# Performance work log

Hardware: AMD Instinct MI355X
Metric: run time of the kernel (lower is better)

Reference implementation:

```python
import jax, jax.numpy as jnp
import numpy as np


def unfold(x, k, pad, stride):
    # x: [B, C, H, W] -> [B, C*k*k, L], matching torch.nn.functional.unfold
    B, C, H, W = x.shape
    p = jax.lax.conv_general_dilated_patches(
        x, (k, k), (stride, stride), [(pad, pad), (pad, pad)],
        dimension_numbers=("NCHW", "OIHW", "NCHW"))  # [B, C*k*k, Lh, Lw]
    return p.reshape(B, C * k * k, -1)


def fold(x, out_hw, k, pad, stride):
    # x: [B, C*k*k, L] -> [B, C, H, W] with overlap-add, matching F.fold
    B, F, L = x.shape
    C = F // (k * k)
    H, W = out_hw
    Hp, Wp = H + 2 * pad, W + 2 * pad
    Lh = (Hp - k) // stride + 1
    Lw = (Wp - k) // stride + 1
    v = x.reshape(B, C, k, k, Lh, Lw)
    rows = jnp.arange(k)[:, None] + jnp.arange(Lh)[None, :] * stride  # [k, Lh]
    cols = jnp.arange(k)[:, None] + jnp.arange(Lw)[None, :] * stride  # [k, Lw]
    idx = rows[:, None, :, None] * Wp + cols[None, :, None, :]        # [k, k, Lh, Lw]
    out = jnp.zeros((B, C, Hp * Wp), x.dtype)
    out = out.at[:, :, idx.reshape(-1)].add(v.reshape(B, C, -1))
    out = out.reshape(B, C, Hp, Wp)
    return out[:, :, pad:pad + H, pad:pad + W]


def setup_inputs() -> dict:
    key = jax.random.key(0)
    k1, k2, k3 = jax.random.split(key, 3)
    B, C, H, W = 2, 16, 96, 96
    return {
        "lrsr_lv1": jax.random.normal(k1, (B, C, H, W), jnp.float32),
        "refsr_lv1": jax.random.normal(k2, (B, C, H, W), jnp.float32),
        "org": jax.random.normal(k3, (B, C, 2 * H, 2 * W), jnp.float32),
        "kernel_size": 3,
        "padding": 1,
        "stride": 1,
        "lv": 2,
    }


def reference(lrsr_lv1, refsr_lv1, org, kernel_size, padding, stride, lv):
    k, pad, s = kernel_size, padding, stride
    eps = 1e-12  # F.normalize default eps
    lr_u = unfold(lrsr_lv1, k, pad, s)                       # [B, F, L]
    ref_u = unfold(refsr_lv1, k, pad, s).transpose(0, 2, 1)  # [B, L, F]
    ref_n = ref_u / jnp.maximum(
        jnp.sqrt(jnp.sum(ref_u * ref_u, axis=2, keepdims=True)), eps)
    lr_n = lr_u / jnp.maximum(
        jnp.sqrt(jnp.sum(lr_u * lr_u, axis=1, keepdims=True)), eps)
    R = jnp.einsum("blf,bfm->blm", ref_n, lr_n)              # [B, L_ref, L_lr]
    S = jnp.argmax(R, axis=1)                                 # [B, L_lr] int
    lv_ = max(lv - 1, 0)
    sc = 2 ** lv_
    k2, p2, s2 = sc * k, sc * pad, sc * s
    org_u = unfold(org, k2, p2, s2)                           # [B, F_org, L]
    T_u = jnp.take_along_axis(org_u, S[:, None, :], axis=2)   # bis gather
    H2 = lrsr_lv1.shape[2] * sc
    W2 = lrsr_lv1.shape[3] * sc
    T_org = fold(T_u, (H2, W2), k2, p2, s2)
    return T_org, S
```

## Files before the change

kernel.cpp:

```cpp
#include <hip/hip_runtime.h>
#include <float.h>


#define BATCH 2
#define CCH   16
#define HH    96
#define WW    96
#define LP    9216
#define KF    144
#define K3    160
#define OH    192
#define OW    192
#define NRT2  36
#define NCB2  36

typedef _Float16 f16;
typedef __attribute__((ext_vector_type(8))) _Float16 f16x8;
typedef __attribute__((ext_vector_type(4))) float    f32x4;

__device__ __forceinline__ void async16(const void* g, void* l) {
    __builtin_amdgcn_global_load_lds(
        (const __attribute__((address_space(1))) void*)g,
        (__attribute__((address_space(3))) void*)l, 16, 0, 0);
}

__global__ __launch_bounds__(256) void k_pack2(
        const float* __restrict__ ref, const float* __restrict__ lr,
        float* __restrict__ rinv, float* __restrict__ bns,
        f16* __restrict__ Abig, f16* __restrict__ Bbig) {
    __shared__ float imgS[CCH][3][26];
    __shared__ float pnorm[24][8];
    __shared__ float scl[24];
    int py = blockIdx.x, b = blockIdx.y;
    int side = blockIdx.z >> 2, q = blockIdx.z & 3;
    int tid = threadIdx.x;
    const float* img = (side ? lr : ref) + (size_t)b * CCH * HH * WW;

    for (int i = tid; i < CCH * 3 * 26; i += 256) {
        int c = i / 78, rem = i - c * 78;
        int rr = rem / 26, xx = rem - rr * 26;
        int y = py + rr - 1, xi = q * 24 - 1 + xx;
        float v = 0.f;
        if ((unsigned)y < (unsigned)HH && (unsigned)xi < (unsigned)WW)
            v = img[(c * HH + y) * WW + xi];
        imgS[c][rr][xx] = v;
    }
    __syncthreads();

    if (tid < 192) {
        int pxl = tid >> 3, part = tid & 7;
        float s = 0.f;
        #pragma unroll
        for (int cc = 0; cc < 2; ++cc) {
            int c = part * 2 + cc;
            #pragma unroll
            for (int dy = 0; dy < 3; ++dy)
                #pragma unroll
                for (int dx = 0; dx < 3; ++dx) {
                    float v = imgS[c][dy][pxl + dx];
                    s += v * v;
                }
        }
        pnorm[pxl][part] = s;
    }
    __syncthreads();

    if (tid < 24) {
        int pxl = tid;
        float s = 0.f;
        #pragma unroll
        for (int p = 0; p < 8; ++p) s += pnorm[pxl][p];
        int gl = b * LP + py * 96 + q * 24 + pxl;
        if (side) { bns[gl] = 1024.0f * sqrtf(s); scl[pxl] = 1024.0f; }
        else { float r = 1.0f / fmaxf(sqrtf(s), 1e-12f); rinv[gl] = r; scl[pxl] = 1024.0f * r; }
    }
    __syncthreads();

    f16* dstb = (side ? Bbig : Abig) + (size_t)(b * LP + py * 96 + q * 24) * K3;
    for (int i = tid; i < 24 * 20; i += 256) {
        int pxl = i / 20, g = i - pxl * 20;
        int f0 = g * 8;
        float sc = scl[pxl];
        f16x8 o;
        #pragma unroll
        for (int e = 0; e < 8; ++e) {
            int f = f0 + e;
            float v = 0.f;
            if (f < KF) {
                int c = f / 9, r9 = f - c * 9;
                int dy = r9 / 3, dx = r9 - dy * 3;
                v = imgS[c][dy][pxl + dx] * sc;
            }
            o[e] = (f16)v;
        }
        *(f16x8*)(dstb + (size_t)pxl * K3 + g * 8) = o;
    }
}

__global__ __launch_bounds__(1024) void k_mfma(
        const f16* __restrict__ Abig, const f16* __restrict__ Bbig,
        float* __restrict__ pv1, int* __restrict__ pi1, float* __restrict__ pv2) {
    __shared__ f16 smem[2][256 * 64];
    int tid = threadIdx.x, lane = tid & 63, w = tid >> 6;
    int wm = w & 3, wn = w >> 2;
    int l15 = lane & 15, quad = lane >> 4;

    int i = blockIdx.x;
    int xcd = i & 7, slot = i >> 3;
    int cb = slot / 9;
    int brt = xcd * 9 + (slot - cb * 9);
    int b = brt / NRT2, rt = brt - b * NRT2;
    int r0 = rt * 256, c0 = cb * 256;

    int ri  = ((lane >> 3) << 1) | ((lane >> 2) & 1);
    int qsw = (lane & 3) ^ ((lane >> 3) & 3);
    const f16* gsrc[2];
    int ldsbyte[2];
    #pragma unroll
    for (int j = 0; j < 2; ++j) {
        int G = w * 2 + j;
        int row8 = G * 16 + ri;
        const f16* base = (row8 < 256)
            ? Abig + (size_t)(b * LP + r0 + row8) * K3
            : Bbig + (size_t)(b * LP + c0 + (row8 - 256)) * K3;
        gsrc[j] = base + qsw * 8;
        ldsbyte[j] = G * 1024;
    }
    int l2 = l15 >> 1, lo1 = l15 & 1;
    int gsel = (quad ^ (l2 & 3)) * 16;
    int abyte[4], bbyte[4];
    #pragma unroll
    for (int t = 0; t < 4; ++t) {
        abyte[t] = (wm * 32 + t * 8 + l2) * 128 + lo1 * 64 + gsel;
        bbyte[t] = (128 + wn * 32 + t * 8 + l2) * 128 + lo1 * 64 + gsel;
    }

    f32x4 acc[4][4];
    #pragma unroll
    for (int ii = 0; ii < 4; ++ii)
        #pragma unroll
        for (int j = 0; j < 4; ++j) { acc[ii][j][0]=0.f; acc[ii][j][1]=0.f; acc[ii][j][2]=0.f; acc[ii][j][3]=0.f; }

    #pragma unroll
    for (int j = 0; j < 2; ++j) async16(gsrc[j], (char*)smem[0] + ldsbyte[j]);

    for (int ch = 0; ch < 5; ++ch) {
        __syncthreads();
        if (ch < 4) {
            #pragma unroll
            for (int j = 0; j < 2; ++j)
                async16(gsrc[j] + (ch + 1) * 32, (char*)smem[(ch + 1) & 1] + ldsbyte[j]);
        }
        const char* buf = (const char*)smem[ch & 1];
        f16x8 af[4], bf[4];
        #pragma unroll
        for (int t = 0; t < 4; ++t) af[t] = *(const f16x8*)(buf + abyte[t]);
        #pragma unroll
        for (int t = 0; t < 4; ++t) bf[t] = *(const f16x8*)(buf + bbyte[t]);
        #pragma unroll
        for (int rtt = 0; rtt < 4; ++rtt)
            #pragma unroll
            for (int ct = 0; ct < 4; ++ct)
                acc[rtt][ct] = __builtin_amdgcn_mfma_f32_16x16x32_f16(af[rtt], bf[ct], acc[rtt][ct], 0, 0, 0);
    }
    __syncthreads();

    float* sv1 = (float*)smem;
    int*   si1 = (int*)  ((char*)smem + 4096);
    float* sv2 = (float*)((char*)smem + 8192);

    int rbase = r0 + wm * 64 + (quad << 2);
    #pragma unroll
    for (int ct = 0; ct < 4; ++ct) {
        float v1 = -FLT_MAX, v2 = -FLT_MAX; int i1 = 0;
        #pragma unroll
        for (int rtt = 0; rtt < 4; ++rtt)
            #pragma unroll
            for (int e = 0; e < 4; ++e) {
                float v = acc[rtt][ct][e];
                int rg = rbase + rtt * 16 + e;
                if (v > v1) { v2 = v1; v1 = v; i1 = rg; }
                else if (v > v2) v2 = v;
            }
        #pragma unroll
        for (int off = 16; off < 64; off <<= 1) {
            float ov1 = __shfl_xor(v1, off, 64);
            int   oi1 = __shfl_xor(i1, off, 64);
            float ov2 = __shfl_xor(v2, off, 64);
            if (ov1 > v1 || (ov1 == v1 && oi1 < i1)) { v2 = fmaxf(v1, ov2); v1 = ov1; i1 = oi1; }
            else v2 = fmaxf(v2, ov1);
        }
        if (quad == 0) {
            int col = wn * 64 + ct * 16 + l15;
            sv1[wm * 256 + col] = v1; si1[wm * 256 + col] = i1; sv2[wm * 256 + col] = v2;
        }
    }
    __syncthreads();
    if (tid < 256) {
        int col = tid;
        float v1 = sv1[col]; int i1 = si1[col]; float v2 = sv2[col];
        #pragma unroll
        for (int m = 1; m < 4; ++m) {
            float ov1 = sv1[m * 256 + col]; int oi1 = si1[m * 256 + col]; float ov2 = sv2[m * 256 + col];
            if (ov1 > v1) { v2 = fmaxf(v1, ov2); v1 = ov1; i1 = oi1; }
            else v2 = fmaxf(v2, ov1);
        }
        size_t o = ((size_t)(b * NRT2 + rt)) * LP + c0 + col;
        pv1[o] = v1; pi1[o] = i1; pv2[o] = v2;
    }
}

__global__ __launch_bounds__(256) void k_merge(
        const float* __restrict__ pv1, const int* __restrict__ pi1,
        const float* __restrict__ pv2, const float* __restrict__ bns,
        int* __restrict__ Sint, float* __restrict__ Sout,
        int* __restrict__ flaglist, int* __restrict__ nflag) {
    int b = blockIdx.y;
    int col = blockIdx.x * 256 + threadIdx.x;
    int gid = b * LP + col;
    float v1 = -FLT_MAX, v2 = -FLT_MAX; int i1 = 0;
    for (int rc = 0; rc < NRT2; ++rc) {
        size_t o = ((size_t)(b * NRT2 + rc)) * LP + col;
        float cv1 = pv1[o]; int ci1 = pi1[o]; float cv2 = pv2[o];
        if (cv1 > v1) { v2 = fmaxf(v1, cv2); v1 = cv1; i1 = ci1; }
        else v2 = fmaxf(v2, cv1);
    }
    Sint[gid] = i1;
    Sout[gid] = (float)i1;
    float tau = bns[gid] * 0.5f;
    if (v1 - v2 < tau) {
        int k = atomicAdd(nflag, 1);
        flaglist[k] = gid;
    }
}

__global__ __launch_bounds__(256) void k_fix(
        const float* __restrict__ refimg, const float* __restrict__ lrimg,
        const float* __restrict__ rinv, const float* __restrict__ pv1,
        const float* __restrict__ bns,
        const int* __restrict__ flaglist, const int* __restrict__ nflag,
        int* __restrict__ Sint, float* __restrict__ Sout) {
    __shared__ float bcol[KF];
    __shared__ float spv[NRT2];
    __shared__ float red[4]; __shared__ int redi[4];
    int tid = threadIdx.x;
    int nf = *nflag;
    for (int fi = blockIdx.x; fi < nf; fi += gridDim.x) {
        int gid = flaglist[fi];
        int b = gid / LP, col = gid - b * LP;
        int lh = col / 96, lw = col - lh * 96;
        __syncthreads();
        if (tid < KF) {
            int c = tid / 9, r = tid - c * 9;
            int dy = r / 3, dx = r - dy * 3;
            int y = lh + dy - 1, x = lw + dx - 1;
            float v = 0.f;
            if ((unsigned)y < (unsigned)HH && (unsigned)x < (unsigned)WW)
                v = lrimg[((size_t)(b * CCH + c) * HH + y) * WW + x];
            bcol[tid] = v;
        }
        if (tid < NRT2) spv[tid] = pv1[((size_t)(b * NRT2 + tid)) * LP + col];
        __syncthreads();
        float v1 = -FLT_MAX;
        for (int rc = 0; rc < NRT2; ++rc) v1 = fmaxf(v1, spv[rc]);
        float thresh = v1 - bns[gid] * 0.5f;
        float best = -FLT_MAX; int bi = 0x7fffffff;
        for (int rc = 0; rc < NRT2; ++rc) {
            if (spv[rc] < thresh) continue;
            int row = rc * 256 + tid;
            int py = row / WW, px = row - py * WW;
            float s = 0.f;
            for (int c = 0; c < CCH; ++c) {
                const float* ic = refimg + (size_t)(b * CCH + c) * HH * WW;
                #pragma unroll
                for (int dy = 0; dy < 3; ++dy) {
                    int y = py + dy - 1;
                    if ((unsigned)y >= (unsigned)HH) continue;
                    #pragma unroll
                    for (int dx = 0; dx < 3; ++dx) {
                        int x = px + dx - 1;
                        if ((unsigned)x >= (unsigned)WW) continue;
                        s = fmaf(ic[y * WW + x], bcol[c * 9 + dy * 3 + dx], s);
                    }
                }
            }
            s *= rinv[b * LP + row];
            if (s > best || (s == best && row < bi)) { best = s; bi = row; }
        }
        #pragma unroll
        for (int off = 1; off < 64; off <<= 1) {
            float ov = __shfl_xor(best, off, 64);
            int   oi = __shfl_xor(bi, off, 64);
            if (ov > best || (ov == best && oi < bi)) { best = ov; bi = oi; }
        }
        if ((tid & 63) == 0) { red[tid >> 6] = best; redi[tid >> 6] = bi; }
        __syncthreads();
        if (tid == 0) {
            float b0 = red[0]; int i0 = redi[0];
            for (int k = 1; k < 4; ++k)
                if (red[k] > b0 || (red[k] == b0 && redi[k] < i0)) { b0 = red[k]; i0 = redi[k]; }
            Sint[gid] = i0;
            Sout[gid] = (float)i0;
        }
    }
}

__global__ __launch_bounds__(256) void k_fold(
        const int* __restrict__ Sint, const float* __restrict__ org,
        float* __restrict__ outT) {
    __shared__ int s_S[6][6];
    int tx = blockIdx.x, ty = blockIdx.y, b = blockIdx.z;
    int x0 = tx * 8, y0 = ty * 8;
    int lhb = 4 * ty - 1; if (lhb < 0) lhb = 0;
    int lwb = 4 * tx - 1; if (lwb < 0) lwb = 0;
    int lhe = 4 * ty + 4; if (lhe > 95) lhe = 95;
    int lwe = 4 * tx + 4; if (lwe > 95) lwe = 95;
    int nh = lhe - lhb + 1, nw = lwe - lwb + 1;
    int tid = threadIdx.x;

    if (tid < 36) {
        int ph = tid / 6, pw = tid - ph * 6;
        int lh = lhb + ph, lw = lwb + pw;
        s_S[ph][pw] = (lh <= lhe && lw <= lwe) ? Sint[b * LP + lh * 96 + lw] : 0;
    }
    __syncthreads();

    int wid = tid >> 6, pix = tid & 63;
    int pyL = pix >> 3, pxL = pix & 7;
    int y = y0 + pyL, x = x0 + pxL;
    const float* orgb = org + ((size_t)b * CCH + wid * 4) * OH * OW;
    float acc[4];
    #pragma unroll
    for (int c = 0; c < 4; ++c) acc[c] = 0.f;
    for (int ph = 0; ph < nh; ++ph) {
        int lh = lhb + ph;
        int dy = y + 2 - 2 * lh;
        for (int pw = 0; pw < nw; ++pw) {
            int lw = lwb + pw;
            int dx = x + 2 - 2 * lw;
            int s  = s_S[ph][pw];
            int sh = s / 96, sw = s - sh * 96;
            if ((unsigned)dy < 6u && (unsigned)dx < 6u) {
                int u = 2 * sh + dy - 2;
                int v = 2 * sw + dx - 2;
                if ((unsigned)u < (unsigned)OH && (unsigned)v < (unsigned)OW) {
                    const float* p = orgb + u * OW + v;
                    #pragma unroll
                    for (int c = 0; c < 4; ++c) acc[c] += p[(size_t)c * OH * OW];
                }
            }
        }
    }
    #pragma unroll
    for (int c = 0; c < 4; ++c)
        outT[(((size_t)(b * CCH + wid * 4 + c)) * OH + y) * OW + x] = acc[c];
}

extern "C" void kernel_launch(void* const* d_in, const int* in_sizes, int n_in,
                              void* d_out, int out_size, void* d_ws, size_t ws_size,
                              hipStream_t stream) {
    const float* lrsr  = (const float*)d_in[0];
    const float* refsr = (const float*)d_in[1];
    const float* org   = (const float*)d_in[2];

    char* ws = (char*)d_ws;
    size_t o = 0;
    float* rinv     = (float*)(ws + o); o += (size_t)BATCH * LP * 4;
    float* bns      = (float*)(ws + o); o += (size_t)BATCH * LP * 4;
    float* pv1      = (float*)(ws + o); o += (size_t)BATCH * NRT2 * LP * 4;
    int*   pi1      = (int*)  (ws + o); o += (size_t)BATCH * NRT2 * LP * 4;
    float* pv2      = (float*)(ws + o); o += (size_t)BATCH * NRT2 * LP * 4;
    f16*   Abig     = (f16*)  (ws + o); o += (size_t)BATCH * LP * K3 * 2;
    f16*   Bbig     = (f16*)  (ws + o); o += (size_t)BATCH * LP * K3 * 2;
    int*   Sint     = (int*)  (ws + o); o += (size_t)BATCH * LP * 4;
    int*   flaglist = (int*)  (ws + o); o += (size_t)BATCH * LP * 4;
    int*   nflag    = (int*)  (ws + o); o += 16;

    float* outT = (float*)d_out;
    float* outS = outT + (size_t)BATCH * CCH * OH * OW;

    hipMemsetAsync(nflag, 0, 4, stream);
    k_pack2<<<dim3(96, BATCH, 8), 256, 0, stream>>>(refsr, lrsr, rinv, bns, Abig, Bbig);
    k_mfma<<<dim3(NCB2 * NRT2 * BATCH), 1024, 0, stream>>>(Abig, Bbig, pv1, pi1, pv2);
    k_merge<<<dim3(LP / 256, BATCH), 256, 0, stream>>>(pv1, pi1, pv2, bns,
                                                       Sint, outS, flaglist, nflag);
    k_fix<<<dim3(768), 256, 0, stream>>>(refsr, lrsr, rinv, pv1, bns,
                                         flaglist, nflag, Sint, outS);
    k_fold<<<dim3(24, 24, BATCH), 256, 0, stream>>>(Sint, org, outT);
}
```

Measured before the change: 292.9 us.

## Process two row tiles per block, keeping the B tile resident in LDS

Each k_mfma block now computes two consecutive 256-row tiles against the same 256-column B tile. The full B tile (all five K chunks) is kept in LDS, and the A chunks are streamed through a double buffer that prefetches across the tile boundary. The grid is halved to 1296 blocks. The aim is to cut redundant global and L2 loads of B and amortize block launch and prologue cost. The trade-offs are more LDS per block (about 108KB) and fewer blocks, which may hurt occupancy and lose the previous XCD-aware block mapping.

```diff
diff --git a/kernel.cpp b/kernel.cpp
--- a/kernel.cpp
+++ b/kernel.cpp
@@ -100,113 +100,116 @@
 __global__ __launch_bounds__(1024) void k_mfma(
         const f16* __restrict__ Abig, const f16* __restrict__ Bbig,
         float* __restrict__ pv1, int* __restrict__ pi1, float* __restrict__ pv2) {
-    __shared__ f16 smem[2][256 * 64];
+    __shared__ f16 smem[2][8192];
+    __shared__ f16 bsm[5][8192];
+    __shared__ float scr[3072];
     int tid = threadIdx.x, lane = tid & 63, w = tid >> 6;
     int wm = w & 3, wn = w >> 2;
     int l15 = lane & 15, quad = lane >> 4;
 
-    int i = blockIdx.x;
-    int xcd = i & 7, slot = i >> 3;
-    int cb = slot / 9;
-    int brt = xcd * 9 + (slot - cb * 9);
-    int b = brt / NRT2, rt = brt - b * NRT2;
-    int r0 = rt * 256, c0 = cb * 256;
+    int bid = blockIdx.x;
+    int rg = bid % 18;
+    int cb = (bid / 18) % 36;
+    int b  = bid / 648;
+    int c0 = cb * 256;
 
     int ri  = ((lane >> 3) << 1) | ((lane >> 2) & 1);
     int qsw = (lane & 3) ^ ((lane >> 3) & 3);
-    const f16* gsrc[2];
-    int ldsbyte[2];
-    #pragma unroll
-    for (int j = 0; j < 2; ++j) {
-        int G = w * 2 + j;
-        int row8 = G * 16 + ri;
-        const f16* base = (row8 < 256)
-            ? Abig + (size_t)(b * LP + r0 + row8) * K3
-            : Bbig + (size_t)(b * LP + c0 + (row8 - 256)) * K3;
-        gsrc[j] = base + qsw * 8;
-        ldsbyte[j] = G * 1024;
-    }
+    const f16* bsrc = Bbig + (size_t)(b * LP + c0 + w * 16 + ri) * K3 + qsw * 8;
+    int ldsoff = w * 1024;
+
     int l2 = l15 >> 1, lo1 = l15 & 1;
     int gsel = (quad ^ (l2 & 3)) * 16;
     int abyte[4], bbyte[4];
     #pragma unroll
     for (int t = 0; t < 4; ++t) {
         abyte[t] = (wm * 32 + t * 8 + l2) * 128 + lo1 * 64 + gsel;
-        bbyte[t] = (128 + wn * 32 + t * 8 + l2) * 128 + lo1 * 64 + gsel;
-    }
-
-    f32x4 acc[4][4];
-    #pragma unroll
-    for (int ii = 0; ii < 4; ++ii)
-        #pragma unroll
-        for (int j = 0; j < 4; ++j) { acc[ii][j][0]=0.f; acc[ii][j][1]=0.f; acc[ii][j][2]=0.f; acc[ii][j][3]=0.f; }
-
-    #pragma unroll
-    for (int j = 0; j < 2; ++j) async16(gsrc[j], (char*)smem[0] + ldsbyte[j]);
-
-    for (int ch = 0; ch < 5; ++ch) {
-        __syncthreads();
-        if (ch < 4) {
-            #pragma unroll
-            for (int j = 0; j < 2; ++j)
-                async16(gsrc[j] + (ch + 1) * 32, (char*)smem[(ch + 1) & 1] + ldsbyte[j]);
-        }
-        const char* buf = (const char*)smem[ch & 1];
-        f16x8 af[4], bf[4];
-        #pragma unroll
-        for (int t = 0; t < 4; ++t) af[t] = *(const f16x8*)(buf + abyte[t]);
-        #pragma unroll
-        for (int t = 0; t < 4; ++t) bf[t] = *(const f16x8*)(buf + bbyte[t]);
-        #pragma unroll
-        for (int rtt = 0; rtt < 4; ++rtt)
-            #pragma unroll
-            for (int ct = 0; ct < 4; ++ct)
-                acc[rtt][ct] = __builtin_amdgcn_mfma_f32_16x16x32_f16(af[rtt], bf[ct], acc[rtt][ct], 0, 0, 0);
-    }
-    __syncthreads();
-
-    float* sv1 = (float*)smem;
-    int*   si1 = (int*)  ((char*)smem + 4096);
-    float* sv2 = (float*)((char*)smem + 8192);
-
-    int rbase = r0 + wm * 64 + (quad << 2);
-    #pragma unroll
-    for (int ct = 0; ct < 4; ++ct) {
-        float v1 = -FLT_MAX, v2 = -FLT_MAX; int i1 = 0;
-        #pragma unroll
-        for (int rtt = 0; rtt < 4; ++rtt)
-            #pragma unroll
-            for (int e = 0; e < 4; ++e) {
-                float v = acc[rtt][ct][e];
-                int rg = rbase + rtt * 16 + e;
-                if (v > v1) { v2 = v1; v1 = v; i1 = rg; }
-                else if (v > v2) v2 = v;
-            }
-        #pragma unroll
-        for (int off = 16; off < 64; off <<= 1) {
-            float ov1 = __shfl_xor(v1, off, 64);
-            int   oi1 = __shfl_xor(i1, off, 64);
-            float ov2 = __shfl_xor(v2, off, 64);
-            if (ov1 > v1 || (ov1 == v1 && oi1 < i1)) { v2 = fmaxf(v1, ov2); v1 = ov1; i1 = oi1; }
-            else v2 = fmaxf(v2, ov1);
-        }
-        if (quad == 0) {
-            int col = wn * 64 + ct * 16 + l15;
-            sv1[wm * 256 + col] = v1; si1[wm * 256 + col] = i1; sv2[wm * 256 + col] = v2;
-        }
-    }
-    __syncthreads();
-    if (tid < 256) {
-        int col = tid;
-        float v1 = sv1[col]; int i1 = si1[col]; float v2 = sv2[col];
-        #pragma unroll
-        for (int m = 1; m < 4; ++m) {
-            float ov1 = sv1[m * 256 + col]; int oi1 = si1[m * 256 + col]; float ov2 = sv2[m * 256 + col];
-            if (ov1 > v1) { v2 = fmaxf(v1, ov2); v1 = ov1; i1 = oi1; }
-            else v2 = fmaxf(v2, ov1);
-        }
-        size_t o = ((size_t)(b * NRT2 + rt)) * LP + c0 + col;
-        pv1[o] = v1; pi1[o] = i1; pv2[o] = v2;
+        bbyte[t] = (wn * 32 + t * 8 + l2) * 128 + lo1 * 64 + gsel;
+    }
+
+    const f16* asrc0 = Abig + (size_t)(b * LP + rg * 512 + w * 16 + ri) * K3 + qsw * 8;
+    async16(asrc0, (char*)smem[0] + ldsoff);
+    async16(bsrc, (char*)bsm[0] + ldsoff);
+
+    for (int rt2 = 0; rt2 < 2; ++rt2) {
+        int rt = rg * 2 + rt2;
+        int r0 = rt * 256;
+        const f16* asrc = asrc0 + (size_t)rt2 * 256 * K3;
+
+        f32x4 acc[4][4];
+        #pragma unroll
+        for (int ii = 0; ii < 4; ++ii)
+            #pragma unroll
+            for (int j = 0; j < 4; ++j) { acc[ii][j][0]=0.f; acc[ii][j][1]=0.f; acc[ii][j][2]=0.f; acc[ii][j][3]=0.f; }
+
+        for (int ch = 0; ch < 5; ++ch) {
+            int g = rt2 * 5 + ch;
+            __syncthreads();
+            if (ch < 4) {
+                async16(asrc + (ch + 1) * 32, (char*)smem[(g + 1) & 1] + ldsoff);
+                if (rt2 == 0)
+                    async16(bsrc + (ch + 1) * 32, (char*)bsm[ch + 1] + ldsoff);
+            } else if (rt2 == 0) {
+                async16(asrc + 256 * K3, (char*)smem[(g + 1) & 1] + ldsoff);
+            }
+            const char* abuf = (const char*)smem[g & 1];
+            const char* bbuf = (const char*)bsm[ch];
+            f16x8 af[4], bf[4];
+            #pragma unroll
+            for (int t = 0; t < 4; ++t) af[t] = *(const f16x8*)(abuf + abyte[t]);
+            #pragma unroll
+            for (int t = 0; t < 4; ++t) bf[t] = *(const f16x8*)(bbuf + bbyte[t]);
+            #pragma unroll
+            for (int rtt = 0; rtt < 4; ++rtt)
+                #pragma unroll
+                for (int ct = 0; ct < 4; ++ct)
+                    acc[rtt][ct] = __builtin_amdgcn_mfma_f32_16x16x32_f16(af[rtt], bf[ct], acc[rtt][ct], 0, 0, 0);
+        }
+        __syncthreads();
+
+        float* sv1 = scr;
+        int*   si1 = (int*)(scr + 1024);
+        float* sv2 = scr + 2048;
+
+        int rbase = r0 + wm * 64 + (quad << 2);
+        #pragma unroll
+        for (int ct = 0; ct < 4; ++ct) {
+            float v1 = -FLT_MAX, v2 = -FLT_MAX; int i1 = 0;
+            #pragma unroll
+            for (int rtt = 0; rtt < 4; ++rtt)
+                #pragma unroll
+                for (int e = 0; e < 4; ++e) {
+                    float v = acc[rtt][ct][e];
+                    int rg2 = rbase + rtt * 16 + e;
+                    if (v > v1) { v2 = v1; v1 = v; i1 = rg2; }
+                    else if (v > v2) v2 = v;
+                }
+            #pragma unroll
+            for (int off = 16; off < 64; off <<= 1) {
+                float ov1 = __shfl_xor(v1, off, 64);
+                int   oi1 = __shfl_xor(i1, off, 64);
+                float ov2 = __shfl_xor(v2, off, 64);
+                if (ov1 > v1 || (ov1 == v1 && oi1 < i1)) { v2 = fmaxf(v1, ov2); v1 = ov1; i1 = oi1; }
+                else v2 = fmaxf(v2, ov1);
+            }
+            if (quad == 0) {
+                int col = wn * 64 + ct * 16 + l15;
+                sv1[wm * 256 + col] = v1; si1[wm * 256 + col] = i1; sv2[wm * 256 + col] = v2;
+            }
+        }
+        __syncthreads();
+        if (tid < 256) {
+            int col = tid;
+            float v1 = sv1[col]; int i1 = si1[col]; float v2 = sv2[col];
+            #pragma unroll
+            for (int m = 1; m < 4; ++m) {
+                float ov1 = sv1[m * 256 + col]; int oi1 = si1[m * 256 + col]; float ov2 = sv2[m * 256 + col];
+                if (ov1 > v1) { v2 = fmaxf(v1, ov2); v1 = ov1; i1 = oi1; }
+                else v2 = fmaxf(v2, ov1);
+            }
+            size_t o = ((size_t)(b * NRT2 + rt)) * LP + c0 + col;
+            pv1[o] = v1; pi1[o] = i1; pv2[o] = v2;
+        }
     }
 }
 
@@ -381,7 +384,7 @@
 
     hipMemsetAsync(nflag, 0, 4, stream);
     k_pack2<<<dim3(96, BATCH, 8), 256, 0, stream>>>(refsr, lrsr, rinv, bns, Abig, Bbig);
-    k_mfma<<<dim3(NCB2 * NRT2 * BATCH), 1024, 0, stream>>>(Abig, Bbig, pv1, pi1, pv2);
+    k_mfma<<<dim3(1296), 1024, 0, stream>>>(Abig, Bbig, pv1, pi1, pv2);
     k_merge<<<dim3(LP / 256, BATCH), 256, 0, stream>>>(pv1, pi1, pv2, bns,
                                                        Sint, outS, flaglist, nflag);
     k_fix<<<dim3(768), 256, 0, stream>>>(refsr, lrsr, rinv, pv1, bns,
```

Result: slower. 309.8 us (+5.8%).

## Pre-tile packed operands and load MFMA fragments directly from global memory

Applied to the files above, without the earlier changes.

The pack kernel now writes A and B operands in a chunk-tiled layout (per 256-row tile, per 32-element K chunk), so each wave can load its MFMA fragments with contiguous 16-byte global loads. The GEMM kernel drops the LDS double-buffered async staging and per-chunk barriers and reads fragments straight from global/L2. This removes LDS traffic and synchronisation, but every wave now re-reads shared tiles from cache with no load-compute overlap beyond what the compiler schedules.

```diff
diff --git a/kernel.cpp b/kernel.cpp
--- a/kernel.cpp
+++ b/kernel.cpp
@@ -13,16 +13,11 @@
 #define OW    192
 #define NRT2  36
 #define NCB2  36
+#define CHELE 8192
 
 typedef _Float16 f16;
 typedef __attribute__((ext_vector_type(8))) _Float16 f16x8;
 typedef __attribute__((ext_vector_type(4))) float    f32x4;
-
-__device__ __forceinline__ void async16(const void* g, void* l) {
-    __builtin_amdgcn_global_load_lds(
-        (const __attribute__((address_space(1))) void*)g,
-        (__attribute__((address_space(3))) void*)l, 16, 0, 0);
-}
 
 __global__ __launch_bounds__(256) void k_pack2(
         const float* __restrict__ ref, const float* __restrict__ lr,
@@ -76,9 +71,12 @@
     }
     __syncthreads();
 
-    f16* dstb = (side ? Bbig : Abig) + (size_t)(b * LP + py * 96 + q * 24) * K3;
+    f16* dst0 = (side ? Bbig : Abig) + (size_t)b * NRT2 * 5 * CHELE;
     for (int i = tid; i < 24 * 20; i += 256) {
         int pxl = i / 20, g = i - pxl * 20;
+        int gr = py * 96 + q * 24 + pxl;
+        int rt = gr >> 8, rr = gr & 255;
+        int ch = g >> 2, g4 = g & 3;
         int f0 = g * 8;
         float sc = scl[pxl];
         f16x8 o;
@@ -93,14 +91,14 @@
             }
             o[e] = (f16)v;
         }
-        *(f16x8*)(dstb + (size_t)pxl * K3 + g * 8) = o;
+        *(f16x8*)(dst0 + ((size_t)rt * 5 + ch) * CHELE + (rr * 4 + g4) * 8) = o;
     }
 }
 
 __global__ __launch_bounds__(1024) void k_mfma(
         const f16* __restrict__ Abig, const f16* __restrict__ Bbig,
         float* __restrict__ pv1, int* __restrict__ pi1, float* __restrict__ pv2) {
-    __shared__ f16 smem[2][256 * 64];
+    __shared__ float scr[3072];
     int tid = threadIdx.x, lane = tid & 63, w = tid >> 6;
     int wm = w & 3, wn = w >> 2;
     int l15 = lane & 15, quad = lane >> 4;
@@ -112,27 +110,13 @@
     int b = brt / NRT2, rt = brt - b * NRT2;
     int r0 = rt * 256, c0 = cb * 256;
 
-    int ri  = ((lane >> 3) << 1) | ((lane >> 2) & 1);
-    int qsw = (lane & 3) ^ ((lane >> 3) & 3);
-    const f16* gsrc[2];
-    int ldsbyte[2];
-    #pragma unroll
-    for (int j = 0; j < 2; ++j) {
-        int G = w * 2 + j;
-        int row8 = G * 16 + ri;
-        const f16* base = (row8 < 256)
-            ? Abig + (size_t)(b * LP + r0 + row8) * K3
-            : Bbig + (size_t)(b * LP + c0 + (row8 - 256)) * K3;
-        gsrc[j] = base + qsw * 8;
-        ldsbyte[j] = G * 1024;
-    }
-    int l2 = l15 >> 1, lo1 = l15 & 1;
-    int gsel = (quad ^ (l2 & 3)) * 16;
-    int abyte[4], bbyte[4];
+    const f16* abase = Abig + ((size_t)(b * NRT2 + rt) * 5) * CHELE;
+    const f16* bbase = Bbig + ((size_t)(b * NRT2 + cb) * 5) * CHELE;
+    int aoff[4], boff[4];
     #pragma unroll
     for (int t = 0; t < 4; ++t) {
-        abyte[t] = (wm * 32 + t * 8 + l2) * 128 + lo1 * 64 + gsel;
-        bbyte[t] = (128 + wn * 32 + t * 8 + l2) * 128 + lo1 * 64 + gsel;
+        aoff[t] = ((wm * 64 + t * 16 + l15) * 4 + quad) * 8;
+        boff[t] = ((wn * 64 + t * 16 + l15) * 4 + quad) * 8;
     }
 
     f32x4 acc[4][4];
@@ -141,33 +125,24 @@
         #pragma unroll
         for (int j = 0; j < 4; ++j) { acc[ii][j][0]=0.f; acc[ii][j][1]=0.f; acc[ii][j][2]=0.f; acc[ii][j][3]=0.f; }
 
-    #pragma unroll
-    for (int j = 0; j < 2; ++j) async16(gsrc[j], (char*)smem[0] + ldsbyte[j]);
-
     for (int ch = 0; ch < 5; ++ch) {
-        __syncthreads();
-        if (ch < 4) {
-            #pragma unroll
-            for (int j = 0; j < 2; ++j)
-                async16(gsrc[j] + (ch + 1) * 32, (char*)smem[(ch + 1) & 1] + ldsbyte[j]);
-        }
-        const char* buf = (const char*)smem[ch & 1];
+        const f16* ac = abase + (size_t)ch * CHELE;
+        const f16* bc = bbase + (size_t)ch * CHELE;
         f16x8 af[4], bf[4];
         #pragma unroll
-        for (int t = 0; t < 4; ++t) af[t] = *(const f16x8*)(buf + abyte[t]);
-        #pragma unroll
-        for (int t = 0; t < 4; ++t) bf[t] = *(const f16x8*)(buf + bbyte[t]);
+        for (int t = 0; t < 4; ++t) af[t] = *(const f16x8*)(ac + aoff[t]);
+        #pragma unroll
+        for (int t = 0; t < 4; ++t) bf[t] = *(const f16x8*)(bc + boff[t]);
         #pragma unroll
         for (int rtt = 0; rtt < 4; ++rtt)
             #pragma unroll
             for (int ct = 0; ct < 4; ++ct)
                 acc[rtt][ct] = __builtin_amdgcn_mfma_f32_16x16x32_f16(af[rtt], bf[ct], acc[rtt][ct], 0, 0, 0);
     }
-    __syncthreads();
-
-    float* sv1 = (float*)smem;
-    int*   si1 = (int*)  ((char*)smem + 4096);
-    float* sv2 = (float*)((char*)smem + 8192);
+
+    float* sv1 = scr;
+    int*   si1 = (int*)(scr + 1024);
+    float* sv2 = scr + 2048;
 
     int rbase = r0 + wm * 64 + (quad << 2);
     #pragma unroll
```

Measured after the change: 345.3 us. 17.9% more time.
